# Kernel optimization log

Measured on AMD Instinct MI355X. Metric: run time of the kernel, lower is better.

The kernel has to match this reference:

```python
import jax, jax.numpy as jnp
import numpy as np

D_MODEL, D_FF, N_EXPERTS, TOP_K = 1024, 2048, 8, 2
B, S = 2, 2048

def setup_inputs() -> dict:
    key = jax.random.key(0)
    k1, k2, k3, k4 = jax.random.split(key, 4)
    scale = 0.02
    return {
        "x": jax.random.normal(k1, (B, S, D_MODEL), dtype=jnp.float32),
        "gate_w": jax.random.normal(k2, (D_MODEL, N_EXPERTS), dtype=jnp.float32) * scale,
        "w1": jax.random.normal(k3, (N_EXPERTS, D_MODEL, D_FF), dtype=jnp.float32) * scale,
        "w2": jax.random.normal(k4, (N_EXPERTS, D_FF, D_MODEL), dtype=jnp.float32) * scale,
    }

def reference(x, gate_w, w1, w2):
    # --- Router (eval mode: no exploration noise, no dropout) ---
    router_logits = jnp.einsum('bsd,de->bse', x, gate_w)          # [B,S,E]
    top_logits, top_idx = jax.lax.top_k(router_logits, TOP_K)      # [B,S,K]
    top_w = jax.nn.softmax(top_logits, axis=-1)                    # [B,S,K]
    # topk indices are distinct per token, so per-(token,expert) combine weight
    # is the sum over k of weight_k * 1[idx_k == e] (matches torch gather/argmax logic)
    combine = jnp.sum(
        jax.nn.one_hot(top_idx, N_EXPERTS, dtype=x.dtype) * top_w[..., None],
        axis=-2)                                                   # [B,S,E]
    # --- Experts: dense-compute formulation of the gather/MLP/scatter loop ---
    h = jax.nn.silu(jnp.einsum('bsd,edf->ebsf', x, w1))            # [E,B,S,Dff]
    y = jnp.einsum('ebsf,efd->ebsd', h, w2)                        # [E,B,S,D]
    out = jnp.einsum('ebsd,bse->bsd', y, combine)                  # [B,S,D]
    return out
```

## Files before the change

### kernel.cpp

```cpp
#include <hip/hip_runtime.h>
#include <cstdint>
#include <cstddef>

#define D_MODEL 1024
#define D_FF    2048
#define N_EXP   8
#define NTOK    4096
#define NASSIGN (NTOK * 2)

typedef __bf16 bf16_t;
typedef bf16_t bf16x8 __attribute__((ext_vector_type(8)));
typedef float  f32x4  __attribute__((ext_vector_type(4)));

typedef __attribute__((address_space(3))) void       lds_void;
typedef const __attribute__((address_space(1))) void gl_void;

__device__ __forceinline__ unsigned short f2b(float f) {
  union { float f; unsigned u; } v; v.f = f;
  unsigned u = v.u;
  unsigned r = (u + 0x7FFFu + ((u >> 16) & 1u)) >> 16;
  return (unsigned short)r;
}

__global__ __launch_bounds__(256) void router_k(
    const float* __restrict__ x, const float* __restrict__ gw,
    int* __restrict__ eidx, float* __restrict__ ewt)
{
  const int wv = threadIdx.x >> 6, lane = threadIdx.x & 63;
  const int token = blockIdx.x * 4 + wv;
  const float4* xr4 = (const float4*)(x + (size_t)token * D_MODEL);
  const float4* gw4 = (const float4*)gw;

  float acc[8] = {};
  #pragma unroll
  for (int it = 0; it < 4; ++it) {
    float4 xv = xr4[it * 64 + lane];
    int d0 = it * 256 + lane * 4;
    #pragma unroll
    for (int i = 0; i < 4; ++i) {
      int d = d0 + i;
      float4 g0 = gw4[d * 2];
      float4 g1 = gw4[d * 2 + 1];
      float xs = (i == 0) ? xv.x : (i == 1) ? xv.y : (i == 2) ? xv.z : xv.w;
      acc[0] += xs * g0.x; acc[1] += xs * g0.y;
      acc[2] += xs * g0.z; acc[3] += xs * g0.w;
      acc[4] += xs * g1.x; acc[5] += xs * g1.y;
      acc[6] += xs * g1.z; acc[7] += xs * g1.w;
    }
  }
  #pragma unroll
  for (int m = 1; m < 64; m <<= 1) {
    #pragma unroll
    for (int k = 0; k < 8; ++k) acc[k] += __shfl_xor(acc[k], m);
  }
  if (lane == 0) {
    int i1 = 0; float v1 = acc[0];
    #pragma unroll
    for (int k = 1; k < 8; ++k) if (acc[k] > v1) { v1 = acc[k]; i1 = k; }
    int i2 = -1; float v2 = -1e30f;
    #pragma unroll
    for (int k = 0; k < 8; ++k) if (k != i1 && acc[k] > v2) { v2 = acc[k]; i2 = k; }
    float t  = __expf(v2 - v1);
    float w1 = 1.f / (1.f + t);
    float w2 = t * w1;
    eidx[token * 2 + 0] = i1; eidx[token * 2 + 1] = i2;
    ewt [token * 2 + 0] = w1; ewt [token * 2 + 1] = w2;
  }
}

__global__ __launch_bounds__(1024) void scan_k(
    const int* __restrict__ eidx, const float* __restrict__ ewt,
    int* __restrict__ counts, int* __restrict__ offsets,
    int* __restrict__ rowtok, float* __restrict__ rowwt)
{
  __shared__ int hist[1024][9];
  __shared__ int soff[8];
  const int t = threadIdx.x;

  int myeid[8];
  int pre[8];
  int local[8] = {};
  #pragma unroll
  for (int i = 0; i < 8; ++i) {
    int e = eidx[t * 8 + i];
    myeid[i] = e;
    pre[i] = local[e];
    local[e]++;
  }
  #pragma unroll
  for (int e = 0; e < 8; ++e) hist[t][e] = local[e];
  __syncthreads();

  for (int ofs = 1; ofs < 1024; ofs <<= 1) {
    int v[8];
    if (t >= ofs) {
      #pragma unroll
      for (int e = 0; e < 8; ++e) v[e] = hist[t - ofs][e];
    }
    __syncthreads();
    if (t >= ofs) {
      #pragma unroll
      for (int e = 0; e < 8; ++e) hist[t][e] += v[e];
    }
    __syncthreads();
  }

  if (t == 0) {
    int o = 0;
    for (int e = 0; e < 8; ++e) {
      int c = hist[1023][e];
      counts[e] = c;
      offsets[e] = o;
      soff[e] = o;
      o += c;
    }
  }
  __syncthreads();

  int excl[8];
  #pragma unroll
  for (int e = 0; e < 8; ++e) excl[e] = hist[t][e] - local[e];

  #pragma unroll
  for (int i = 0; i < 8; ++i) {
    int b = t * 8 + i;
    int e = myeid[i];
    int row = soff[e] + excl[e] + pre[i];
    rowtok[row] = b >> 1;
    rowwt[row]  = ewt[b];
  }
}

__global__ __launch_bounds__(256) void gather_k(
    const float* __restrict__ x, const int* __restrict__ rowtok,
    unsigned short* __restrict__ Xe)
{
  const int row = blockIdx.x;
  const int token = rowtok[row];
  const float4* xr = (const float4*)(x + (size_t)token * D_MODEL);
  ushort4* dst = (ushort4*)(Xe + (size_t)row * D_MODEL);
  float4 v = xr[threadIdx.x];
  ushort4 o;
  o.x = f2b(v.x); o.y = f2b(v.y); o.z = f2b(v.z); o.w = f2b(v.w);
  dst[threadIdx.x] = o;
}

__global__ __launch_bounds__(256) void transcvt_k(
    const float* __restrict__ in, unsigned short* __restrict__ out, int R, int C)
{
  __shared__ float T[32][33];
  const int e = blockIdx.z;
  const float* ein = in + (size_t)e * R * C;
  unsigned short* eout = out + (size_t)e * R * C;
  const int c0 = blockIdx.x * 32, r0 = blockIdx.y * 32;
  const int tx = threadIdx.x & 31, ty = threadIdx.x >> 5;
  #pragma unroll
  for (int i = 0; i < 4; ++i) {
    int rr = ty + i * 8;
    T[rr][tx] = ein[(size_t)(r0 + rr) * C + c0 + tx];
  }
  __syncthreads();
  #pragma unroll
  for (int i = 0; i < 4; ++i) {
    int cc = ty + i * 8;
    eout[(size_t)(c0 + cc) * R + r0 + tx] = f2b(T[tx][cc]);
  }
}

template<int K, int N, int MODE>
__global__ __launch_bounds__(256) void moe_gemm_k(
    const unsigned short* __restrict__ A,
    const unsigned short* __restrict__ Bt,
    unsigned short* __restrict__ Hout,
    float* __restrict__ out,
    const int* __restrict__ counts, const int* __restrict__ offsets,
    const int* __restrict__ rowtok, const float* __restrict__ rowwt)
{
  const int e = blockIdx.z;
  const int cnt = counts[e];
  const int m0 = blockIdx.y * 128;
  if (m0 >= cnt) return;
  const int base = offsets[e];
  const int n0 = blockIdx.x * 128;

  __shared__ unsigned short lA[128 * 32];
  __shared__ unsigned short lB[128 * 32];

  const int tid = threadIdx.x;
  const int lane = tid & 63;
  const int wv = tid >> 6;
  const int wm = wv & 1, wn = wv >> 1;
  const int col = lane & 15, quad = lane >> 4;

  const unsigned short* Aseg = A + (size_t)base * K;
  const unsigned short* Bseg = Bt + (size_t)e * ((size_t)N * K);

  f32x4 acc[4][4] = {};

  for (int k0 = 0; k0 < K; k0 += 32) {
    __syncthreads();
    #pragma unroll
    for (int r = 0; r < 2; ++r) {
      int flat = ((r * 4 + wv) * 64 + lane) * 16;
      int row = flat >> 6;
      int kb  = flat & 63;
      const char* gA = (const char*)Aseg + ((size_t)(m0 + row) * K + k0) * 2 + kb;
      const char* gB = (const char*)Bseg + ((size_t)(n0 + row) * K + k0) * 2 + kb;
      char* lpa = (char*)lA + (r * 4 + wv) * 1024;
      char* lpb = (char*)lB + (r * 4 + wv) * 1024;
      __builtin_amdgcn_global_load_lds((gl_void*)gA, (lds_void*)lpa, 16, 0, 0);
      __builtin_amdgcn_global_load_lds((gl_void*)gB, (lds_void*)lpb, 16, 0, 0);
    }
    __syncthreads();

    bf16x8 af[4], bfr[4];
    #pragma unroll
    for (int i = 0; i < 4; ++i)
      af[i] = *(const bf16x8*)(lA + ((wm * 64 + i * 16 + col) * 32 + quad * 8));
    #pragma unroll
    for (int j = 0; j < 4; ++j)
      bfr[j] = *(const bf16x8*)(lB + ((wn * 64 + j * 16 + col) * 32 + quad * 8));
    #pragma unroll
    for (int i = 0; i < 4; ++i)
      #pragma unroll
      for (int j = 0; j < 4; ++j)
        acc[i][j] = __builtin_amdgcn_mfma_f32_16x16x32_bf16(af[i], bfr[j], acc[i][j], 0, 0, 0);
  }

  #pragma unroll
  for (int i = 0; i < 4; ++i) {
    #pragma unroll
    for (int reg = 0; reg < 4; ++reg) {
      int r = m0 + wm * 64 + i * 16 + quad * 4 + reg;
      if (r < cnt) {
        if (MODE == 1) {
          unsigned short* hrow = Hout + (size_t)(base + r) * N + (n0 + wn * 64 + col);
          #pragma unroll
          for (int j = 0; j < 4; ++j) {
            float v = acc[i][j][reg];
            float s = v / (1.f + __expf(-v));
            hrow[j * 16] = f2b(s);
          }
        } else {
          int   token = rowtok[base + r];
          float wgt   = rowwt[base + r];
          float* orow = out + (size_t)token * D_MODEL + (n0 + wn * 64 + col);
          #pragma unroll
          for (int j = 0; j < 4; ++j)
            atomicAdd(&orow[j * 16], wgt * acc[i][j][reg]);
        }
      }
    }
  }
}

extern "C" void kernel_launch(void* const* d_in, const int* in_sizes, int n_in,
                              void* d_out, int out_size, void* d_ws, size_t ws_size,
                              hipStream_t stream) {
  const float* x  = (const float*)d_in[0];
  const float* gw = (const float*)d_in[1];
  const float* w1 = (const float*)d_in[2];
  const float* w2 = (const float*)d_in[3];
  float* out = (float*)d_out;

  char* ws = (char*)d_ws;
  size_t off = 0;
  auto alloc = [&](size_t bytes) -> char* {
    char* p = ws + off; off += (bytes + 255) & ~(size_t)255; return p;
  };
  int*   ctrl    = (int*)alloc(256);
  int*   counts  = ctrl;
  int*   offsets = ctrl + 8;
  int*   eidx    = (int*)  alloc((size_t)NASSIGN * 4);
  float* ewt     = (float*)alloc((size_t)NASSIGN * 4);
  int*   rowtok  = (int*)  alloc((size_t)NASSIGN * 4);
  float* rowwt   = (float*)alloc((size_t)NASSIGN * 4);
  unsigned short* Xe  = (unsigned short*)alloc((size_t)(NASSIGN + 128) * D_MODEL * 2);
  unsigned short* H   = (unsigned short*)alloc((size_t)(NASSIGN + 128) * D_FF * 2);
  unsigned short* w1t = (unsigned short*)alloc((size_t)N_EXP * D_MODEL * D_FF * 2);
  unsigned short* w2t = (unsigned short*)alloc((size_t)N_EXP * D_MODEL * D_FF * 2);

  hipMemsetAsync(d_out, 0, (size_t)out_size * sizeof(float), stream);

  router_k<<<NTOK / 4, 256, 0, stream>>>(x, gw, eidx, ewt);
  scan_k<<<1, 1024, 0, stream>>>(eidx, ewt, counts, offsets, rowtok, rowwt);
  gather_k<<<NASSIGN, 256, 0, stream>>>(x, rowtok, Xe);
  transcvt_k<<<dim3(D_FF / 32, D_MODEL / 32, N_EXP), 256, 0, stream>>>(w1, w1t, D_MODEL, D_FF);
  transcvt_k<<<dim3(D_MODEL / 32, D_FF / 32, N_EXP), 256, 0, stream>>>(w2, w2t, D_FF, D_MODEL);

  moe_gemm_k<D_MODEL, D_FF, 1><<<dim3(D_FF / 128, 32, N_EXP), 256, 0, stream>>>(
      Xe, w1t, H, nullptr, counts, offsets, rowtok, rowwt);
  moe_gemm_k<D_FF, D_MODEL, 2><<<dim3(D_MODEL / 128, 32, N_EXP), 256, 0, stream>>>(
      H, w2t, nullptr, out, counts, offsets, rowtok, rowwt);
}
```

Before: 352.2 us.

## Replace atomic scatter with bf16 expert outputs plus combine kernel; vectorize transpose

The second expert GEMM now writes weighted bf16 rows to a buffer instead of atomically adding into the float output. A new combine kernel sums each token's two expert rows, which removes the output memset and the atomic traffic. The scan kernel now records each assignment's row index and runs on 256 threads with 32 items each. The weight transpose-convert kernel uses 64x64 tiles with float4 loads and ushort4 stores. Rounding expert outputs to bf16 before the sum adds some numeric error, and the combine kernel adds an extra launch and a read and write of the intermediate buffer.

```diff
diff --git a/kernel.cpp b/kernel.cpp
--- a/kernel.cpp
+++ b/kernel.cpp
@@ -20,6 +20,9 @@
   unsigned u = v.u;
   unsigned r = (u + 0x7FFFu + ((u >> 16) & 1u)) >> 16;
   return (unsigned short)r;
+}
+__device__ __forceinline__ float b2f(unsigned short b) {
+  union { unsigned u; float f; } v; v.u = ((unsigned)b) << 16; return v.f;
 }
 
 __global__ __launch_bounds__(256) void router_k(
@@ -68,30 +71,23 @@
   }
 }
 
-__global__ __launch_bounds__(1024) void scan_k(
+__global__ __launch_bounds__(256) void scan_k(
     const int* __restrict__ eidx, const float* __restrict__ ewt,
     int* __restrict__ counts, int* __restrict__ offsets,
-    int* __restrict__ rowtok, float* __restrict__ rowwt)
-{
-  __shared__ int hist[1024][9];
+    int* __restrict__ rowtok, float* __restrict__ rowwt, int* __restrict__ rowof)
+{
+  __shared__ int hist[256][9];
   __shared__ int soff[8];
   const int t = threadIdx.x;
 
-  int myeid[8];
-  int pre[8];
   int local[8] = {};
-  #pragma unroll
-  for (int i = 0; i < 8; ++i) {
-    int e = eidx[t * 8 + i];
-    myeid[i] = e;
-    pre[i] = local[e];
-    local[e]++;
-  }
+  #pragma unroll 4
+  for (int i = 0; i < 32; ++i) local[eidx[t * 32 + i]]++;
   #pragma unroll
   for (int e = 0; e < 8; ++e) hist[t][e] = local[e];
   __syncthreads();
 
-  for (int ofs = 1; ofs < 1024; ofs <<= 1) {
+  for (int ofs = 1; ofs < 256; ofs <<= 1) {
     int v[8];
     if (t >= ofs) {
       #pragma unroll
@@ -108,7 +104,7 @@
   if (t == 0) {
     int o = 0;
     for (int e = 0; e < 8; ++e) {
-      int c = hist[1023][e];
+      int c = hist[255][e];
       counts[e] = c;
       offsets[e] = o;
       soff[e] = o;
@@ -117,17 +113,18 @@
   }
   __syncthreads();
 
-  int excl[8];
-  #pragma unroll
-  for (int e = 0; e < 8; ++e) excl[e] = hist[t][e] - local[e];
-
-  #pragma unroll
-  for (int i = 0; i < 8; ++i) {
-    int b = t * 8 + i;
-    int e = myeid[i];
-    int row = soff[e] + excl[e] + pre[i];
+  int run[8];
+  #pragma unroll
+  for (int e = 0; e < 8; ++e) run[e] = soff[e] + hist[t][e] - local[e];
+
+  #pragma unroll 4
+  for (int i = 0; i < 32; ++i) {
+    int b = t * 32 + i;
+    int e = eidx[b];
+    int row = run[e]++;
     rowtok[row] = b >> 1;
     rowwt[row]  = ewt[b];
+    rowof[b]    = row;
   }
 }
 
@@ -148,22 +145,29 @@
 __global__ __launch_bounds__(256) void transcvt_k(
     const float* __restrict__ in, unsigned short* __restrict__ out, int R, int C)
 {
-  __shared__ float T[32][33];
+  __shared__ float T[64][65];
   const int e = blockIdx.z;
   const float* ein = in + (size_t)e * R * C;
   unsigned short* eout = out + (size_t)e * R * C;
-  const int c0 = blockIdx.x * 32, r0 = blockIdx.y * 32;
-  const int tx = threadIdx.x & 31, ty = threadIdx.x >> 5;
+  const int c0 = blockIdx.x * 64, r0 = blockIdx.y * 64;
+  const int g = threadIdx.x >> 4;
+  const int m = threadIdx.x & 15;
+
   #pragma unroll
   for (int i = 0; i < 4; ++i) {
-    int rr = ty + i * 8;
-    T[rr][tx] = ein[(size_t)(r0 + rr) * C + c0 + tx];
+    int r = i * 16 + g;
+    float4 v = *(const float4*)(ein + (size_t)(r0 + r) * C + c0 + m * 4);
+    T[r][m * 4 + 0] = v.x; T[r][m * 4 + 1] = v.y;
+    T[r][m * 4 + 2] = v.z; T[r][m * 4 + 3] = v.w;
   }
   __syncthreads();
   #pragma unroll
   for (int i = 0; i < 4; ++i) {
-    int cc = ty + i * 8;
-    eout[(size_t)(c0 + cc) * R + r0 + tx] = f2b(T[tx][cc]);
+    int c = i * 16 + g;
+    ushort4 o;
+    o.x = f2b(T[m * 4 + 0][c]); o.y = f2b(T[m * 4 + 1][c]);
+    o.z = f2b(T[m * 4 + 2][c]); o.w = f2b(T[m * 4 + 3][c]);
+    *(ushort4*)(eout + (size_t)(c0 + c) * R + r0 + m * 4) = o;
   }
 }
 
@@ -172,9 +176,8 @@
     const unsigned short* __restrict__ A,
     const unsigned short* __restrict__ Bt,
     unsigned short* __restrict__ Hout,
-    float* __restrict__ out,
     const int* __restrict__ counts, const int* __restrict__ offsets,
-    const int* __restrict__ rowtok, const float* __restrict__ rowwt)
+    const float* __restrict__ rowwt)
 {
   const int e = blockIdx.z;
   const int cnt = counts[e];
@@ -233,8 +236,8 @@
     for (int reg = 0; reg < 4; ++reg) {
       int r = m0 + wm * 64 + i * 16 + quad * 4 + reg;
       if (r < cnt) {
+        unsigned short* hrow = Hout + (size_t)(base + r) * N + (n0 + wn * 64 + col);
         if (MODE == 1) {
-          unsigned short* hrow = Hout + (size_t)(base + r) * N + (n0 + wn * 64 + col);
           #pragma unroll
           for (int j = 0; j < 4; ++j) {
             float v = acc[i][j][reg];
@@ -242,16 +245,32 @@
             hrow[j * 16] = f2b(s);
           }
         } else {
-          int   token = rowtok[base + r];
-          float wgt   = rowwt[base + r];
-          float* orow = out + (size_t)token * D_MODEL + (n0 + wn * 64 + col);
+          float wgt = rowwt[base + r];
           #pragma unroll
           for (int j = 0; j < 4; ++j)
-            atomicAdd(&orow[j * 16], wgt * acc[i][j][reg]);
+            hrow[j * 16] = f2b(wgt * acc[i][j][reg]);
         }
       }
     }
   }
+}
+
+__global__ __launch_bounds__(256) void combine_k(
+    const unsigned short* __restrict__ Y, const int* __restrict__ rowof,
+    float* __restrict__ out)
+{
+  const int token = blockIdx.x;
+  const int r1 = rowof[token * 2];
+  const int r2 = rowof[token * 2 + 1];
+  const int d4 = threadIdx.x;
+  ushort4 a = *(const ushort4*)(Y + (size_t)r1 * D_MODEL + d4 * 4);
+  ushort4 b = *(const ushort4*)(Y + (size_t)r2 * D_MODEL + d4 * 4);
+  float4 o;
+  o.x = b2f(a.x) + b2f(b.x);
+  o.y = b2f(a.y) + b2f(b.y);
+  o.z = b2f(a.z) + b2f(b.z);
+  o.w = b2f(a.w) + b2f(b.w);
+  *(float4*)(out + (size_t)token * D_MODEL + d4 * 4) = o;
 }
 
 extern "C" void kernel_launch(void* const* d_in, const int* in_sizes, int n_in,
@@ -275,21 +294,22 @@
   float* ewt     = (float*)alloc((size_t)NASSIGN * 4);
   int*   rowtok  = (int*)  alloc((size_t)NASSIGN * 4);
   float* rowwt   = (float*)alloc((size_t)NASSIGN * 4);
+  int*   rowof   = (int*)  alloc((size_t)NASSIGN * 4);
   unsigned short* Xe  = (unsigned short*)alloc((size_t)(NASSIGN + 128) * D_MODEL * 2);
   unsigned short* H   = (unsigned short*)alloc((size_t)(NASSIGN + 128) * D_FF * 2);
+  unsigned short* Y   = (unsigned short*)alloc((size_t)(NASSIGN + 128) * D_MODEL * 2);
   unsigned short* w1t = (unsigned short*)alloc((size_t)N_EXP * D_MODEL * D_FF * 2);
   unsigned short* w2t = (unsigned short*)alloc((size_t)N_EXP * D_MODEL * D_FF * 2);
 
-  hipMemsetAsync(d_out, 0, (size_t)out_size * sizeof(float), stream);
-
   router_k<<<NTOK / 4, 256, 0, stream>>>(x, gw, eidx, ewt);
-  scan_k<<<1, 1024, 0, stream>>>(eidx, ewt, counts, offsets, rowtok, rowwt);
+  scan_k<<<1, 256, 0, stream>>>(eidx, ewt, counts, offsets, rowtok, rowwt, rowof);
   gather_k<<<NASSIGN, 256, 0, stream>>>(x, rowtok, Xe);
-  transcvt_k<<<dim3(D_FF / 32, D_MODEL / 32, N_EXP), 256, 0, stream>>>(w1, w1t, D_MODEL, D_FF);
-  transcvt_k<<<dim3(D_MODEL / 32, D_FF / 32, N_EXP), 256, 0, stream>>>(w2, w2t, D_FF, D_MODEL);
+  transcvt_k<<<dim3(D_FF / 64, D_MODEL / 64, N_EXP), 256, 0, stream>>>(w1, w1t, D_MODEL, D_FF);
+  transcvt_k<<<dim3(D_MODEL / 64, D_FF / 64, N_EXP), 256, 0, stream>>>(w2, w2t, D_FF, D_MODEL);
 
   moe_gemm_k<D_MODEL, D_FF, 1><<<dim3(D_FF / 128, 32, N_EXP), 256, 0, stream>>>(
-      Xe, w1t, H, nullptr, counts, offsets, rowtok, rowwt);
+      Xe, w1t, H, counts, offsets, rowwt);
   moe_gemm_k<D_FF, D_MODEL, 2><<<dim3(D_MODEL / 128, 32, N_EXP), 256, 0, stream>>>(
-      H, w2t, nullptr, out, counts, offsets, rowtok, rowwt);
-}
+      H, w2t, Y, counts, offsets, rowwt);
+  combine_k<<<NTOK, 256, 0, stream>>>(Y, rowof, out);
+}
```

Result: no change. 348.9 us (-0.9%).
